# Kernel optimization log

Hardware: AMD Instinct MI355X
Metric: run time of the kernel (lower is better)

Reference implementation:

```python
import jax, jax.numpy as jnp
import numpy as np

B, H, W, C = 32, 64, 64, 512
NH, WIN, SHIFT = 16, 8, 4
S = WIN * WIN           # tokens per window = 64
HD = C // NH            # head dim = 32
FF = 4 * C
EPS = 1e-5
NW = (H // WIN) * (W // WIN)  # windows per image = 64


def _build_attn_mask():
    # Static shifted-window mask, same construction as SwinBlock_tp.__init__
    img = np.zeros((H, W), np.float32)
    slices = (slice(0, -WIN), slice(-WIN, -SHIFT), slice(-SHIFT, None))
    cnt = 0
    for hs in slices:
        for ws in slices:
            img[hs, ws] = cnt
            cnt += 1
    # window_partition on (1,H,W,1)
    m = img.reshape(H // WIN, WIN, W // WIN, WIN).transpose(0, 2, 1, 3).reshape(-1, S)
    diff = m[:, None, :] - m[:, :, None]            # (NW, S, S)
    return jnp.asarray(diff != 0)[:, None, :, :]     # (NW, 1, S, S) bool, True = masked

_ATTN_MASK = _build_attn_mask()


def _layernorm(x, g, b):
    mu = jnp.mean(x, axis=-1, keepdims=True)
    var = jnp.var(x, axis=-1, keepdims=True)
    return (x - mu) * jax.lax.rsqrt(var + EPS) * g + b


def _window_partition(x):
    # (B,H,W,C) -> (B*NW, S, C)
    x = x.reshape(B, H // WIN, WIN, W // WIN, WIN, C)
    x = x.transpose(0, 1, 3, 2, 4, 5)
    return x.reshape(-1, S, C)


def _window_reverse(x):
    # (B*NW, S, C) -> (B,H,W,C)
    x = x.reshape(B, H // WIN, W // WIN, WIN, WIN, C)
    x = x.transpose(0, 1, 3, 2, 4, 5)
    return x.reshape(B, H, W, C)


def setup_inputs() -> dict:
    key = jax.random.key(0)
    ks = jax.random.split(key, 8)
    sd = 0.02
    return {
        "hidden_states": jax.random.normal(ks[0], (B, H * W, C), jnp.float32),
        "Wqkv": jax.random.normal(ks[1], (C, 3 * C), jnp.float32) * sd,
        "bqkv": jnp.zeros((3 * C,), jnp.float32),
        "Wo": jax.random.normal(ks[2], (C, C), jnp.float32) * sd,
        "bo": jnp.zeros((C,), jnp.float32),
        "ln1_g": jnp.ones((C,), jnp.float32),
        "ln1_b": jnp.zeros((C,), jnp.float32),
        "ln2_g": jnp.ones((C,), jnp.float32),
        "ln2_b": jnp.zeros((C,), jnp.float32),
        "W1": jax.random.normal(ks[3], (C, FF), jnp.float32) * sd,
        "b1": jnp.zeros((FF,), jnp.float32),
        "W2": jax.random.normal(ks[4], (FF, C), jnp.float32) * sd,
        "b2": jnp.zeros((C,), jnp.float32),
    }


def reference(hidden_states, Wqkv, bqkv, Wo, bo, ln1_g, ln1_b, ln2_g, ln2_b, W1, b1, W2, b2):
    shortcut = hidden_states
    x = _layernorm(hidden_states, ln1_g, ln1_b).reshape(B, H, W, C)
    x = jnp.roll(x, shift=(-SHIFT, -SHIFT), axis=(1, 2))
    xw = _window_partition(x)                                  # (B*NW, S, C)

    qkv = xw @ Wqkv + bqkv                                     # (B*NW, S, 3C)
    q, k, v = jnp.split(qkv, 3, axis=-1)
    q = q.reshape(-1, S, NH, HD)
    k = k.reshape(-1, S, NH, HD)
    v = v.reshape(-1, S, NH, HD)
    scale = 1.0 / jnp.sqrt(jnp.float32(HD))
    scores = jnp.einsum("nqhd,nkhd->nhqk", q, k) * scale      # (B*NW, NH, S, S)
    mask = jnp.tile(_ATTN_MASK, (B, 1, 1, 1))                  # (B*NW, 1, S, S)
    scores = jnp.where(mask, -10000.0, scores)
    probs = jax.nn.softmax(scores, axis=-1)
    attn = jnp.einsum("nhqk,nkhd->nqhd", probs, v).reshape(-1, S, C)
    attn = attn @ Wo + bo                                      # out proj (+bias fused)

    x = _window_reverse(attn)
    x = jnp.roll(x, shift=(SHIFT, SHIFT), axis=(1, 2)).reshape(B, H * W, C)
    x = shortcut + x

    y = _layernorm(x, ln2_g, ln2_b)
    y = jax.nn.gelu(y @ W1 + b1, approximate=True) @ W2 + b2
    return x + y
```

## Files before the change

### kernel.cpp

```cpp
#include <hip/hip_runtime.h>
#include <hip/hip_bf16.h>
#include <math.h>

typedef __bf16 bf16_t;
typedef __bf16 bf16x8 __attribute__((ext_vector_type(8)));
typedef float  f32x4  __attribute__((ext_vector_type(4)));

__device__ __forceinline__ int inputs_f32(const unsigned* disc) {
  return disc[0] != 0x3F803F80u;
}

__device__ __forceinline__ float load1(const void* p, size_t i, int f32) {
  return f32 ? ((const float*)p)[i] : (float)((const bf16_t*)p)[i];
}

__device__ __forceinline__ void load_lds16(const bf16_t* g, bf16_t* l) {
  __builtin_amdgcn_global_load_lds(
      (const __attribute__((address_space(1))) void*)g,
      (__attribute__((address_space(3))) void*)l, 16, 0, 0);
}

__device__ __forceinline__ int region_of(int wh, int ww, int s) {
  int i = s >> 3, j = s & 7;
  int h = wh * 8 + i, w = ww * 8 + j;
  int rh = (h < 56) ? 0 : (h < 60 ? 1 : 2);
  int rw = (w < 56) ? 0 : (w < 60 ? 1 : 2);
  return rh * 3 + rw;
}

__global__ __launch_bounds__(256) void transpose_cvt(const void* __restrict__ in,
                                                     bf16_t* __restrict__ out, int R, int C,
                                                     const unsigned* __restrict__ disc) {
  int f32 = inputs_f32(disc);
  __shared__ bf16_t tile[32][33];
  int tc = blockIdx.x * 32, tr = blockIdx.y * 32;
  int tx = threadIdx.x & 31, ty = threadIdx.x >> 5;
  for (int rr = ty; rr < 32; rr += 8)
    tile[rr][tx] = (bf16_t)load1(in, (size_t)(tr + rr) * C + tc + tx, f32);
  __syncthreads();
  for (int rr = ty; rr < 32; rr += 8)
    out[(size_t)(tc + rr) * R + tr + tx] = tile[tx][rr];
}

__global__ void cvt_vec(const void* __restrict__ src, bf16_t* __restrict__ dst, int n,
                        const unsigned* __restrict__ disc) {
  int f32 = inputs_f32(disc);
  int i = blockIdx.x * 256 + threadIdx.x;
  if (i < n) dst[i] = (bf16_t)load1(src, i, f32);
}

template<int PERM>
__global__ __launch_bounds__(256) void ln_kernel(const void* __restrict__ x,
                                                 const bf16_t* __restrict__ g,
                                                 const bf16_t* __restrict__ b,
                                                 bf16_t* __restrict__ out,
                                                 int row0,
                                                 const unsigned* __restrict__ disc) {
  int f32 = PERM ? inputs_f32(disc) : 0;
  int wave = threadIdx.x >> 6, lane = threadIdx.x & 63;
  int r = blockIdx.x * 4 + wave;
  size_t srcrow;
  if (PERM) {
    int bi = r >> 12, nw = (r >> 6) & 63, s = r & 63;
    int wh = nw >> 3, ww = nw & 7, ii = s >> 3, jj = s & 7;
    int h = (wh * 8 + ii + 4) & 63, w = (ww * 8 + jj + 4) & 63;
    srcrow = (size_t)row0 + ((bi << 12) | (h << 6) | w);
  } else {
    srcrow = (size_t)r;
  }
  float f[8];
  if (f32) {
    const float* fp = (const float*)x + srcrow * 512 + lane * 8;
    float4 a = ((const float4*)fp)[0], c = ((const float4*)fp)[1];
    f[0]=a.x; f[1]=a.y; f[2]=a.z; f[3]=a.w; f[4]=c.x; f[5]=c.y; f[6]=c.z; f[7]=c.w;
  } else {
    bf16x8 v = *(const bf16x8*)((const bf16_t*)x + srcrow * 512 + lane * 8);
#pragma unroll
    for (int k = 0; k < 8; ++k) f[k] = (float)v[k];
  }
  float sum = 0.f;
#pragma unroll
  for (int k = 0; k < 8; ++k) sum += f[k];
#pragma unroll
  for (int off = 1; off < 64; off <<= 1) sum += __shfl_xor(sum, off);
  float mu = sum * (1.0f / 512.0f);
  float sq = 0.f;
#pragma unroll
  for (int k = 0; k < 8; ++k) { float d = f[k] - mu; sq += d * d; }
#pragma unroll
  for (int off = 1; off < 64; off <<= 1) sq += __shfl_xor(sq, off);
  float rstd = rsqrtf(sq * (1.0f / 512.0f) + 1e-5f);
  bf16x8 gv = *(const bf16x8*)(g + lane * 8);
  bf16x8 bv = *(const bf16x8*)(b + lane * 8);
  bf16x8 ov;
#pragma unroll
  for (int k = 0; k < 8; ++k)
    ov[k] = (bf16_t)((f[k] - mu) * rstd * (float)gv[k] + (float)bv[k]);
  *(bf16x8*)(out + (size_t)r * 512 + lane * 8) = ov;
}

__device__ __forceinline__ float gelu_f(float x) {
  float t = tanhf(0.7978845608028654f * (x + 0.044715f * x * x * x));
  return 0.5f * x * (1.0f + t);
}

template<int MODE>
__global__ __launch_bounds__(256) void gemm_bt(const bf16_t* __restrict__ A,
                                               const bf16_t* __restrict__ Bt,
                                               const bf16_t* __restrict__ bias,
                                               const void* extra_raw,
                                               const bf16_t* extra_bf,
                                               void* out_raw,
                                               bf16_t* out_bf,
                                               int row0,
                                               const unsigned* __restrict__ disc,
                                               int N, int K) {
  int f32 = (MODE == 1 || MODE == 3) ? inputs_f32(disc) : 0;
  __shared__ __align__(16) bf16_t As[2 * 128 * 32];
  __shared__ __align__(16) bf16_t Bs[2 * 128 * 32];
  int ntiles = N >> 7;
  int cpx = gridDim.x >> 3;
  int swz = ((int)blockIdx.x & 7) * cpx + ((int)blockIdx.x >> 3);
  int mtile = swz / ntiles, ntile = swz % ntiles;
  int tid = threadIdx.x, lane = tid & 63, wave = tid >> 6;
  int moff = (wave >> 1) * 64, noff = (wave & 1) * 64;
  int quad = lane >> 4, l15 = lane & 15;
  const bf16_t* Ab = A + (size_t)mtile * 128 * K;
  const bf16_t* Bb = Bt + (size_t)ntile * 128 * K;

  auto stage = [&](int buf, int k0) {
#pragma unroll
    for (int cc = 0; cc < 2; ++cc) {
      int c = tid + cc * 256;
      int row = c >> 2, ko = (c & 3) * 8;
      bf16_t* lA = As + buf * 4096 + (size_t)(wave * 64 + cc * 256) * 8;
      bf16_t* lB = Bs + buf * 4096 + (size_t)(wave * 64 + cc * 256) * 8;
      load_lds16(Ab + (size_t)row * K + k0 + ko, lA);
      load_lds16(Bb + (size_t)row * K + k0 + ko, lB);
    }
  };

  f32x4 acc[4][4] = {};
  stage(0, 0);
  __syncthreads();
  int cur = 0;
  for (int k0 = 0; k0 < K; k0 += 32) {
    if (k0 + 32 < K) stage(cur ^ 1, k0 + 32);
    const bf16_t* Ac = As + cur * 4096;
    const bf16_t* Bc = Bs + cur * 4096;
    bf16x8 af[4], bff[4];
#pragma unroll
    for (int t = 0; t < 4; ++t) {
      af[t]  = *(const bf16x8*)(Ac + (moff + t * 16 + l15) * 32 + quad * 8);
      bff[t] = *(const bf16x8*)(Bc + (noff + t * 16 + l15) * 32 + quad * 8);
    }
#pragma unroll
    for (int mt = 0; mt < 4; ++mt)
#pragma unroll
      for (int nt = 0; nt < 4; ++nt)
        acc[mt][nt] = __builtin_amdgcn_mfma_f32_16x16x32_bf16(af[mt], bff[nt], acc[mt][nt], 0, 0, 0);
    __syncthreads();
    cur ^= 1;
  }
#pragma unroll
  for (int mt = 0; mt < 4; ++mt) {
#pragma unroll
    for (int nt = 0; nt < 4; ++nt) {
      int gn = (ntile << 7) + noff + nt * 16 + l15;
      float bi = (float)bias[gn];
#pragma unroll
      for (int i = 0; i < 4; ++i) {
        int gm = (mtile << 7) + moff + mt * 16 + quad * 4 + i;
        float v = acc[mt][nt][i] + bi;
        if (MODE == 2) v = gelu_f(v);
        if (MODE == 0 || MODE == 2) {
          out_bf[(size_t)gm * N + gn] = (bf16_t)v;
        } else if (MODE == 1) {
          int bimg = gm >> 12, nw = (gm >> 6) & 63, s = gm & 63;
          int wh = nw >> 3, ww = nw & 7, ii = s >> 3, jj = s & 7;
          int h = (wh * 8 + ii + 4) & 63, w = (ww * 8 + jj + 4) & 63;
          int t = (bimg << 12) | (h << 6) | w;
          v += load1(extra_raw, ((size_t)row0 + t) * 512 + gn, f32);
          out_bf[(size_t)t * 512 + gn] = (bf16_t)v;
        } else {
          v += (float)extra_bf[(size_t)gm * 512 + gn];
          size_t oidx = ((size_t)row0 + gm) * 512 + gn;
          if (f32) ((float*)out_raw)[oidx] = v;
          else     ((bf16_t*)out_raw)[oidx] = (bf16_t)v;
        }
      }
    }
  }
}

__global__ __launch_bounds__(64) void attn_scalar(const bf16_t* __restrict__ qkv,
                                                  bf16_t* __restrict__ attn_out) {
  __shared__ float Ks[64][33];
  __shared__ float Vs[64][33];
  int win = blockIdx.x >> 4, head = blockIdx.x & 15;
  int nw = win & 63, wh = nw >> 3, ww = nw & 7;
  const bf16_t* base = qkv + (size_t)win * 64 * 1536 + head * 32;
  int t = threadIdx.x;
  const bf16_t* krow = base + 512 + (size_t)t * 1536;
  const bf16_t* vrow = base + 1024 + (size_t)t * 1536;
#pragma unroll
  for (int i = 0; i < 4; ++i) {
    bf16x8 kv = *(const bf16x8*)(krow + i * 8);
    bf16x8 vv = *(const bf16x8*)(vrow + i * 8);
#pragma unroll
    for (int j = 0; j < 8; ++j) { Ks[t][i * 8 + j] = (float)kv[j]; Vs[t][i * 8 + j] = (float)vv[j]; }
  }
  __syncthreads();

  float q[32];
  const bf16_t* qrow = base + (size_t)t * 1536;
#pragma unroll
  for (int i = 0; i < 4; ++i) {
    bf16x8 qv = *(const bf16x8*)(qrow + i * 8);
#pragma unroll
    for (int j = 0; j < 8; ++j) q[i * 8 + j] = (float)qv[j];
  }

  const float scale = 0.17677669529663687f;
  int rr = region_of(wh, ww, t);
  float sc[64];
  float mx = -1e30f;
#pragma unroll
  for (int k = 0; k < 64; ++k) {
    float s = 0.f;
#pragma unroll
    for (int d = 0; d < 32; ++d) s += q[d] * Ks[k][d];
    s *= scale;
    if (region_of(wh, ww, k) != rr) s = -10000.0f;
    sc[k] = s;
    mx = fmaxf(mx, s);
  }
  float sum = 0.f;
#pragma unroll
  for (int k = 0; k < 64; ++k) { sc[k] = __expf(sc[k] - mx); sum += sc[k]; }
  float inv = 1.0f / sum;
  float o[32];
#pragma unroll
  for (int d = 0; d < 32; ++d) o[d] = 0.f;
#pragma unroll
  for (int k = 0; k < 64; ++k) {
    float p = sc[k] * inv;
#pragma unroll
    for (int d = 0; d < 32; ++d) o[d] += p * Vs[k][d];
  }
  bf16_t* orow = attn_out + (size_t)win * 64 * 512 + (size_t)t * 512 + head * 32;
#pragma unroll
  for (int i = 0; i < 4; ++i) {
    bf16x8 ov;
#pragma unroll
    for (int j = 0; j < 8; ++j) ov[j] = (bf16_t)o[i * 8 + j];
    *(bf16x8*)(orow + i * 8) = ov;
  }
}

extern "C" void kernel_launch(void* const* d_in, const int* in_sizes, int n_in,
                              void* d_out, int out_size, void* d_ws, size_t ws_size,
                              hipStream_t stream) {
  (void)in_sizes; (void)n_in; (void)out_size; (void)ws_size;
  const void* hidden = d_in[0];
  const void* Wqkv = d_in[1];  const void* bqkv = d_in[2];
  const void* Wo   = d_in[3];  const void* bo   = d_in[4];
  const void* ln1g = d_in[5];  const void* ln1b = d_in[6];
  const void* ln2g = d_in[7];  const void* ln2b = d_in[8];
  const void* W1   = d_in[9];  const void* b1   = d_in[10];
  const void* W2   = d_in[11]; const void* b2   = d_in[12];
  const unsigned* disc = (const unsigned*)d_in[5];
  char* ws = (char*)d_ws;

  bf16_t* WqkvT = (bf16_t*)ws;
  bf16_t* WoT   = WqkvT + 1536 * 512;
  bf16_t* W1T   = WoT + 512 * 512;
  bf16_t* W2T   = W1T + 2048 * 512;
  bf16_t* cbqkv = W2T + 2048 * 512;
  bf16_t* cbo   = cbqkv + 1536;
  bf16_t* cb1   = cbo + 512;
  bf16_t* cb2   = cb1 + 2048;
  bf16_t* cl1g  = cb2 + 512;
  bf16_t* cl1b  = cl1g + 512;
  bf16_t* cl2g  = cl1b + 512;
  bf16_t* cl2b  = cl2g + 512;
  bf16_t* R1 = (bf16_t*)(ws + 0x00800000ULL);
  bf16_t* R2 = (bf16_t*)(ws + 0x02800000ULL);
  bf16_t* R3 = (bf16_t*)(ws + 0x0A800000ULL);
  bf16_t* R4 = (bf16_t*)(ws + 0x0C800000ULL);

  transpose_cvt<<<dim3(48, 16), 256, 0, stream>>>(Wqkv, WqkvT, 512, 1536, disc);
  transpose_cvt<<<dim3(16, 16), 256, 0, stream>>>(Wo, WoT, 512, 512, disc);
  transpose_cvt<<<dim3(64, 16), 256, 0, stream>>>(W1, W1T, 512, 2048, disc);
  transpose_cvt<<<dim3(16, 64), 256, 0, stream>>>(W2, W2T, 2048, 512, disc);
  cvt_vec<<<6, 256, 0, stream>>>(bqkv, cbqkv, 1536, disc);
  cvt_vec<<<2, 256, 0, stream>>>(bo, cbo, 512, disc);
  cvt_vec<<<8, 256, 0, stream>>>(b1, cb1, 2048, disc);
  cvt_vec<<<2, 256, 0, stream>>>(b2, cb2, 512, disc);
  cvt_vec<<<2, 256, 0, stream>>>(ln1g, cl1g, 512, disc);
  cvt_vec<<<2, 256, 0, stream>>>(ln1b, cl1b, 512, disc);
  cvt_vec<<<2, 256, 0, stream>>>(ln2g, cl2g, 512, disc);
  cvt_vec<<<2, 256, 0, stream>>>(ln2b, cl2b, 512, disc);

  for (int c = 0; c < 4; ++c) {
    int row0 = c * 32768;
    bf16_t* xw    = R1;
    bf16_t* qkvc  = R2;
    bf16_t* attnO = R1;
    bf16_t* xresc = R3;
    bf16_t* xln2c = R4;
    bf16_t* ffnh  = R2;
    ln_kernel<1><<<8192, 256, 0, stream>>>(hidden, cl1g, cl1b, xw, row0, disc);
    gemm_bt<0><<<3072, 256, 0, stream>>>(xw, WqkvT, cbqkv, nullptr, nullptr, nullptr, qkvc,
                                         0, disc, 1536, 512);
    attn_scalar<<<8192, 64, 0, stream>>>(qkvc, attnO);
    gemm_bt<1><<<1024, 256, 0, stream>>>(attnO, WoT, cbo, hidden, nullptr, nullptr, xresc,
                                         row0, disc, 512, 512);
    ln_kernel<0><<<8192, 256, 0, stream>>>(xresc, cl2g, cl2b, xln2c, 0, disc);
    gemm_bt<2><<<4096, 256, 0, stream>>>(xln2c, W1T, cb1, nullptr, nullptr, nullptr, ffnh,
                                         0, disc, 2048, 512);
    gemm_bt<3><<<1024, 256, 0, stream>>>(ffnh, W2T, cb2, nullptr, xresc, d_out, nullptr,
                                         row0, disc, 512, 2048);
  }
}
```

Baseline: 2.749 ms.

## Use 256x256 GEMM tiles with a 4-stage swizzled LDS pipeline

The bf16 MFMA GEMM moves from 128x128 tiles with 256 threads and double buffering to 256x256 tiles with 512 threads. It now keeps four K-slices in flight through global_load_lds with explicit vmcnt waits and raw barriers. LDS rows are stored with an XOR chunk swizzle to cut bank conflicts, and the MFMA section runs under raised wave priority. The aim is to raise operand reuse per LDS load and hide global memory latency better. In exchange it uses 128KB of LDS per block and launches fewer blocks, which for the N=512 GEMMs fills only one wave of CUs.

```diff
diff --git a/kernel.cpp b/kernel.cpp
--- a/kernel.cpp
+++ b/kernel.cpp
@@ -105,73 +105,101 @@
 }
 
 template<int MODE>
-__global__ __launch_bounds__(256) void gemm_bt(const bf16_t* __restrict__ A,
-                                               const bf16_t* __restrict__ Bt,
-                                               const bf16_t* __restrict__ bias,
-                                               const void* extra_raw,
-                                               const bf16_t* extra_bf,
-                                               void* out_raw,
-                                               bf16_t* out_bf,
-                                               int row0,
-                                               const unsigned* __restrict__ disc,
-                                               int N, int K) {
+__global__ __launch_bounds__(512, 2) void gemm_bt(const bf16_t* __restrict__ A,
+                                                  const bf16_t* __restrict__ Bt,
+                                                  const bf16_t* __restrict__ bias,
+                                                  const void* extra_raw,
+                                                  const bf16_t* extra_bf,
+                                                  void* out_raw,
+                                                  bf16_t* out_bf,
+                                                  int row0,
+                                                  const unsigned* __restrict__ disc,
+                                                  int N, int K) {
   int f32 = (MODE == 1 || MODE == 3) ? inputs_f32(disc) : 0;
-  __shared__ __align__(16) bf16_t As[2 * 128 * 32];
-  __shared__ __align__(16) bf16_t Bs[2 * 128 * 32];
-  int ntiles = N >> 7;
+  __shared__ __align__(16) bf16_t lds[65536];
+  int ntiles = N >> 8;
   int cpx = gridDim.x >> 3;
   int swz = ((int)blockIdx.x & 7) * cpx + ((int)blockIdx.x >> 3);
   int mtile = swz / ntiles, ntile = swz % ntiles;
   int tid = threadIdx.x, lane = tid & 63, wave = tid >> 6;
-  int moff = (wave >> 1) * 64, noff = (wave & 1) * 64;
+  int wm = wave >> 2, wn = wave & 3;
   int quad = lane >> 4, l15 = lane & 15;
-  const bf16_t* Ab = A + (size_t)mtile * 128 * K;
-  const bf16_t* Bb = Bt + (size_t)ntile * 128 * K;
-
-  auto stage = [&](int buf, int k0) {
-#pragma unroll
-    for (int cc = 0; cc < 2; ++cc) {
-      int c = tid + cc * 256;
-      int row = c >> 2, ko = (c & 3) * 8;
-      bf16_t* lA = As + buf * 4096 + (size_t)(wave * 64 + cc * 256) * 8;
-      bf16_t* lB = Bs + buf * 4096 + (size_t)(wave * 64 + cc * 256) * 8;
-      load_lds16(Ab + (size_t)row * K + k0 + ko, lA);
-      load_lds16(Bb + (size_t)row * K + k0 + ko, lB);
+  const bf16_t* Ab = A + (size_t)mtile * 256 * K;
+  const bf16_t* Bb = Bt + (size_t)ntile * 256 * K;
+  int NT = K >> 5;
+
+  int rowq = tid >> 2;
+  int cchunk = (tid & 3) ^ ((tid >> 3) & 3);
+  int coff = cchunk * 8;
+  int wbase = wave * 512;
+
+  auto stage = [&](int t) {
+    int slot = t & 3;
+    bf16_t* sl = lds + slot * 16384;
+#pragma unroll
+    for (int i = 0; i < 2; ++i) {
+      const bf16_t* gA = Ab + (size_t)(i * 128 + rowq) * K + t * 32 + coff;
+      const bf16_t* gB = Bb + (size_t)(i * 128 + rowq) * K + t * 32 + coff;
+      load_lds16(gA, sl + i * 4096 + wbase);
+      load_lds16(gB, sl + 8192 + i * 4096 + wbase);
     }
   };
 
-  f32x4 acc[4][4] = {};
-  stage(0, 0);
-  __syncthreads();
-  int cur = 0;
-  for (int k0 = 0; k0 < K; k0 += 32) {
-    if (k0 + 32 < K) stage(cur ^ 1, k0 + 32);
-    const bf16_t* Ac = As + cur * 4096;
-    const bf16_t* Bc = Bs + cur * 4096;
-    bf16x8 af[4], bff[4];
-#pragma unroll
-    for (int t = 0; t < 4; ++t) {
-      af[t]  = *(const bf16x8*)(Ac + (moff + t * 16 + l15) * 32 + quad * 8);
-      bff[t] = *(const bf16x8*)(Bc + (noff + t * 16 + l15) * 32 + quad * 8);
-    }
-#pragma unroll
-    for (int mt = 0; mt < 4; ++mt)
-#pragma unroll
-      for (int nt = 0; nt < 4; ++nt)
-        acc[mt][nt] = __builtin_amdgcn_mfma_f32_16x16x32_bf16(af[mt], bff[nt], acc[mt][nt], 0, 0, 0);
-    __syncthreads();
-    cur ^= 1;
-  }
-#pragma unroll
-  for (int mt = 0; mt < 4; ++mt) {
-#pragma unroll
-    for (int nt = 0; nt < 4; ++nt) {
-      int gn = (ntile << 7) + noff + nt * 16 + l15;
+  f32x4 acc[8][4] = {};
+  stage(0); stage(1); stage(2);
+
+  for (int t = 0; t < NT; ++t) {
+    int rem = NT - t;
+    if (rem > 3) {
+      stage(t + 3);
+      asm volatile("s_waitcnt vmcnt(12)" ::: "memory");
+    } else if (rem == 3) {
+      asm volatile("s_waitcnt vmcnt(8)" ::: "memory");
+    } else if (rem == 2) {
+      asm volatile("s_waitcnt vmcnt(4)" ::: "memory");
+    } else {
+      asm volatile("s_waitcnt vmcnt(0)" ::: "memory");
+    }
+    asm volatile("s_barrier" ::: "memory");
+
+    const bf16_t* Asl = lds + (t & 3) * 16384;
+    const bf16_t* Bsl = Asl + 8192;
+    bf16x8 bfr[4];
+#pragma unroll
+    for (int nf = 0; nf < 4; ++nf) {
+      int r = wn * 64 + nf * 16 + l15;
+      bfr[nf] = *(const bf16x8*)(Bsl + r * 32 + ((quad ^ ((r >> 1) & 3)) << 3));
+    }
+#pragma unroll
+    for (int mh = 0; mh < 2; ++mh) {
+      bf16x8 afr[4];
+#pragma unroll
+      for (int mf = 0; mf < 4; ++mf) {
+        int r = wm * 128 + mh * 64 + mf * 16 + l15;
+        afr[mf] = *(const bf16x8*)(Asl + r * 32 + ((quad ^ ((r >> 1) & 3)) << 3));
+      }
+      __builtin_amdgcn_s_setprio(1);
+#pragma unroll
+      for (int mf = 0; mf < 4; ++mf)
+#pragma unroll
+        for (int nf = 0; nf < 4; ++nf)
+          acc[mh * 4 + mf][nf] =
+              __builtin_amdgcn_mfma_f32_16x16x32_bf16(afr[mf], bfr[nf], acc[mh * 4 + mf][nf], 0, 0, 0);
+      __builtin_amdgcn_s_setprio(0);
+    }
+    asm volatile("s_barrier" ::: "memory");
+  }
+
+#pragma unroll
+  for (int mf = 0; mf < 8; ++mf) {
+#pragma unroll
+    for (int nf = 0; nf < 4; ++nf) {
+      int gn = (ntile << 8) + wn * 64 + nf * 16 + l15;
       float bi = (float)bias[gn];
 #pragma unroll
       for (int i = 0; i < 4; ++i) {
-        int gm = (mtile << 7) + moff + mt * 16 + quad * 4 + i;
-        float v = acc[mt][nt][i] + bi;
+        int gm = (mtile << 8) + wm * 128 + mf * 16 + quad * 4 + i;
+        float v = acc[mf][nf][i] + bi;
         if (MODE == 2) v = gelu_f(v);
         if (MODE == 0 || MODE == 2) {
           out_bf[(size_t)gm * N + gn] = (bf16_t)v;
@@ -311,15 +339,15 @@
     bf16_t* xln2c = R4;
     bf16_t* ffnh  = R2;
     ln_kernel<1><<<8192, 256, 0, stream>>>(hidden, cl1g, cl1b, xw, row0, disc);
-    gemm_bt<0><<<3072, 256, 0, stream>>>(xw, WqkvT, cbqkv, nullptr, nullptr, nullptr, qkvc,
-                                         0, disc, 1536, 512);
+    gemm_bt<0><<<768, 512, 0, stream>>>(xw, WqkvT, cbqkv, nullptr, nullptr, nullptr, qkvc,
+                                        0, disc, 1536, 512);
     attn_scalar<<<8192, 64, 0, stream>>>(qkvc, attnO);
-    gemm_bt<1><<<1024, 256, 0, stream>>>(attnO, WoT, cbo, hidden, nullptr, nullptr, xresc,
-                                         row0, disc, 512, 512);
+    gemm_bt<1><<<256, 512, 0, stream>>>(attnO, WoT, cbo, hidden, nullptr, nullptr, xresc,
+                                        row0, disc, 512, 512);
     ln_kernel<0><<<8192, 256, 0, stream>>>(xresc, cl2g, cl2b, xln2c, 0, disc);
-    gemm_bt<2><<<4096, 256, 0, stream>>>(xln2c, W1T, cb1, nullptr, nullptr, nullptr, ffnh,
+    gemm_bt<2><<<1024, 512, 0, stream>>>(xln2c, W1T, cb1, nullptr, nullptr, nullptr, ffnh,
                                          0, disc, 2048, 512);
-    gemm_bt<3><<<1024, 256, 0, stream>>>(ffnh, W2T, cb2, nullptr, xresc, d_out, nullptr,
-                                         row0, disc, 512, 2048);
-  }
-}
+    gemm_bt<3><<<256, 512, 0, stream>>>(ffnh, W2T, cb2, nullptr, xresc, d_out, nullptr,
+                                        row0, disc, 512, 2048);
+  }
+}
```

After: 2.555 ms. 7.1% less time.
